# Performance work log

Hardware: AMD Instinct MI355X
Metric: run time of the kernel (lower is better)

The kernel has to match this reference:

```python
import jax, jax.numpy as jnp
import numpy as np

B, T, C, H = 4, 2048, 1024, 16
D = C // H  # head dim = 64


def setup_inputs() -> dict:
    key = jax.random.key(0)
    ks = jax.random.split(key, 5)
    s = 1.0 / np.sqrt(C)
    return {
        "x": jax.random.normal(ks[0], (B, T, C), dtype=jnp.float32),
        "Wq": jax.random.normal(ks[1], (C, C), dtype=jnp.float32) * s,
        "bq": jnp.zeros((C,), dtype=jnp.float32),
        "Wk": jax.random.normal(ks[2], (C, C), dtype=jnp.float32) * s,
        "bk": jnp.zeros((C,), dtype=jnp.float32),
        "Wv": jax.random.normal(ks[3], (C, C), dtype=jnp.float32) * s,
        "bv": jnp.zeros((C,), dtype=jnp.float32),
        "Wp": jax.random.normal(ks[4], (C, C), dtype=jnp.float32) * s,
        "bp": jnp.zeros((C,), dtype=jnp.float32),
    }


def reference(x, Wq, bq, Wk, bk, Wv, bv, Wp, bp):
    Bb, Tt, Cc = x.shape
    # QKV projections (torch Linear: y = x @ W.T + b)
    q = (x @ Wq.T + bq).reshape(Bb, Tt, H, D).transpose(0, 2, 1, 3)  # [B,H,T,D]
    k = (x @ Wk.T + bk).reshape(Bb, Tt, H, D).transpose(0, 2, 1, 3)
    v = (x @ Wv.T + bv).reshape(Bb, Tt, H, D).transpose(0, 2, 1, 3)
    att = jnp.einsum("bhqd,bhkd->bhqk", q, k) / jnp.sqrt(jnp.float32(D))
    causal = jnp.tril(jnp.ones((Tt, Tt), dtype=bool))
    att = jnp.where(causal[None, None], att, -jnp.inf)
    att = jax.nn.softmax(att, axis=-1)
    y = jnp.einsum("bhqk,bhkd->bhqd", att, v)  # [B,H,T,D]
    y = y.transpose(0, 2, 1, 3).reshape(Bb, Tt, Cc)
    return y @ Wp.T + bp
```

## Files before the change

### kernel.cpp

```cpp
#include <hip/hip_runtime.h>

typedef unsigned short u16;
typedef unsigned int u32;

typedef __attribute__((ext_vector_type(4))) float f32x4;
typedef __attribute__((ext_vector_type(8))) short bf16x8;


__device__ inline u16 f2b(float f) {
  union { float f; u32 u; } x; x.f = f;
  u32 u = x.u;
  u32 r = (u + 0x7fffu + ((u >> 16) & 1u)) >> 16;
  return (u16)r;
}

__device__ inline u32 cvtpk(float lo, float hi) {
  u32 r;
  asm("v_cvt_pk_bf16_f32 %0, %1, %2" : "=v"(r) : "v"(lo), "v"(hi));
  return r;
}

__device__ inline void gload_lds16(const void* g, void* l) {
  __builtin_amdgcn_global_load_lds(
      (const __attribute__((address_space(1))) u32*)g,
      (__attribute__((address_space(3))) u32*)l, 16, 0, 0);
}


__global__ __launch_bounds__(256) void cvt_all(const float* __restrict__ x,
                                               const float* __restrict__ w0,
                                               const float* __restrict__ w1,
                                               const float* __restrict__ w2,
                                               const float* __restrict__ w3,
                                               u16* __restrict__ xo,
                                               u16* __restrict__ wo) {
  int b = blockIdx.x;
  const float* s;
  u16* d;
  int i;
  if (b < 8192) {
    s = x; d = xo; i = b * 256 + threadIdx.x;
  } else {
    int m = (b - 8192) >> 10;
    s = (m == 0) ? w0 : (m == 1) ? w1 : (m == 2) ? w2 : w3;
    d = wo + (size_t)m * 1048576;
    i = ((b - 8192) & 1023) * 256 + threadIdx.x;
  }
  float4 v = ((const float4*)s)[i];
  ushort4 o;
  o.x = f2b(v.x); o.y = f2b(v.y); o.z = f2b(v.z); o.w = f2b(v.w);
  ((ushort4*)d)[i] = o;
}


__global__ __launch_bounds__(256) void gemm_qkv(const u16* __restrict__ A,
                                                const u16* __restrict__ W,
                                                const float* __restrict__ bq,
                                                const float* __restrict__ bk,
                                                const float* __restrict__ bv,
                                                u16* __restrict__ outQ,
                                                u16* __restrict__ outK,
                                                u16* __restrict__ outVt,
                                                float qscale) {
  __shared__ u16 sA[128 * 32];
  __shared__ u16 sB[128 * 32];

  const int K = 1024;
  const int t = threadIdx.x;
  const int lane = t & 63;
  const int w = t >> 6;
  const int wr = w >> 1, wc = w & 1;
  const int lr = lane & 15, lg = lane >> 4;

  int bid = blockIdx.y * 24 + blockIdx.x;
  int swz = (bid & 7) * 192 + (bid >> 3);
  const int mBase = (swz / 24) * 128;
  const int nBase = (swz % 24) * 128;

  f32x4 zero = {0.f, 0.f, 0.f, 0.f};
  f32x4 acc[4][4];
#pragma unroll
  for (int i = 0; i < 4; ++i)
#pragma unroll
    for (int j = 0; j < 4; ++j) acc[i][j] = zero;

  const int rA = t >> 2;
  const int cA = (t & 3) * 8;

  for (int k0 = 0; k0 < K; k0 += 32) {
#pragma unroll
    for (int i = 0; i < 2; ++i) {
      gload_lds16(A + (size_t)(mBase + i * 64 + rA) * K + k0 + cA,
                  &sA[i * 2048 + t * 8]);
      gload_lds16(W + (size_t)(nBase + i * 64 + rA) * K + k0 + cA,
                  &sB[i * 2048 + t * 8]);
    }
    __syncthreads();

    bf16x8 af[4], bf[4];
#pragma unroll
    for (int i = 0; i < 4; ++i)
      af[i] = *(const bf16x8*)&sA[(wr * 64 + i * 16 + lr) * 32 + lg * 8];
#pragma unroll
    for (int j = 0; j < 4; ++j)
      bf[j] = *(const bf16x8*)&sB[(wc * 64 + j * 16 + lr) * 32 + lg * 8];

#pragma unroll
    for (int i = 0; i < 4; ++i)
#pragma unroll
      for (int j = 0; j < 4; ++j)
        acc[i][j] = __builtin_amdgcn_mfma_f32_16x16x32_bf16(af[i], bf[j],
                                                            acc[i][j], 0, 0, 0);
    __syncthreads();
  }

  const int mode = nBase >> 10;
  const float* bias = (mode == 0) ? bq : (mode == 1) ? bk : bv;

#pragma unroll
  for (int i = 0; i < 4; ++i) {
    int row = mBase + wr * 64 + i * 16 + lg * 4;
    int b = row >> 11, tp = row & 2047;
#pragma unroll
    for (int j = 0; j < 4; ++j) {
      int col = nBase + wc * 64 + j * 16 + lr;
      int ncol = col & 1023;
      int h = ncol >> 6, dd = ncol & 63;
      float bv_ = bias[ncol];
      size_t bhOff = (size_t)(b * 16 + h) * 262144;
      if (mode == 2) {
        ushort4 o;
        o.x = f2b(acc[i][j][0] + bv_);
        o.y = f2b(acc[i][j][1] + bv_);
        o.z = f2b(acc[i][j][2] + bv_);
        o.w = f2b(acc[i][j][3] + bv_);
        *(ushort4*)((char*)outVt + bhOff + (tp >> 6) * 8192 + dd * 128 +
                    ((((tp & 63) >> 3) << 4) ^ ((dd & 7) << 4)) +
                    (tp & 7) * 2) = o;
      } else if (mode == 0) {
#pragma unroll
        for (int r = 0; r < 4; ++r)
          outQ[(((size_t)(b * 16 + h) * 2048) + tp + r) * 64 + dd] =
              f2b((acc[i][j][r] + bv_) * qscale);
      } else {
#pragma unroll
        for (int r = 0; r < 4; ++r) {
          int tt = tp + r;
          *(u16*)((char*)outK + bhOff + (tt >> 6) * 8192 + (tt & 63) * 128 +
                  (((dd >> 3) << 4) ^ ((tt & 7) << 4)) + (dd & 7) * 2) =
              f2b(acc[i][j][r] + bv_);
        }
      }
    }
  }
}


__global__ __launch_bounds__(256) void gemm_proj(const u16* __restrict__ A,
                                                 const u16* __restrict__ W,
                                                 const float* __restrict__ bias,
                                                 float* __restrict__ outF) {
  __shared__ u16 sA[128 * 32];
  __shared__ u16 sB[128 * 32];

  const int K = 1024, N = 1024;
  const int t = threadIdx.x;
  const int lane = t & 63;
  const int w = t >> 6;
  const int wr = w >> 1, wc = w & 1;
  const int lr = lane & 15, lg = lane >> 4;

  int bid = blockIdx.y * 8 + blockIdx.x;
  int swz = (bid & 7) * 64 + (bid >> 3);
  const int mBase = (swz >> 3) * 128;
  const int nBase = (swz & 7) * 128;

  f32x4 zero = {0.f, 0.f, 0.f, 0.f};
  f32x4 acc[4][4];
#pragma unroll
  for (int i = 0; i < 4; ++i)
#pragma unroll
    for (int j = 0; j < 4; ++j) acc[i][j] = zero;

  const int rA = t >> 2;
  const int cA = (t & 3) * 8;

  for (int k0 = 0; k0 < K; k0 += 32) {
#pragma unroll
    for (int i = 0; i < 2; ++i) {
      gload_lds16(A + (size_t)(mBase + i * 64 + rA) * K + k0 + cA,
                  &sA[i * 2048 + t * 8]);
      gload_lds16(W + (size_t)(nBase + i * 64 + rA) * K + k0 + cA,
                  &sB[i * 2048 + t * 8]);
    }
    __syncthreads();

    bf16x8 af[4], bf[4];
#pragma unroll
    for (int i = 0; i < 4; ++i)
      af[i] = *(const bf16x8*)&sA[(wr * 64 + i * 16 + lr) * 32 + lg * 8];
#pragma unroll
    for (int j = 0; j < 4; ++j)
      bf[j] = *(const bf16x8*)&sB[(wc * 64 + j * 16 + lr) * 32 + lg * 8];

#pragma unroll
    for (int i = 0; i < 4; ++i)
#pragma unroll
      for (int j = 0; j < 4; ++j)
        acc[i][j] = __builtin_amdgcn_mfma_f32_16x16x32_bf16(af[i], bf[j],
                                                            acc[i][j], 0, 0, 0);
    __syncthreads();
  }

#pragma unroll
  for (int i = 0; i < 4; ++i) {
    int row = mBase + wr * 64 + i * 16 + lg * 4;
#pragma unroll
    for (int j = 0; j < 4; ++j) {
      int col = nBase + wc * 64 + j * 16 + lr;
      float bv = bias[col];
#pragma unroll
      for (int r = 0; r < 4; ++r)
        outF[(size_t)(row + r) * N + col] = acc[i][j][r] + bv;
    }
  }
}


__global__ __launch_bounds__(512) void attn_fwd(const u16* __restrict__ qg,
                                                const u16* __restrict__ kswz,
                                                const u16* __restrict__ vswz,
                                                u16* __restrict__ yg) {
  __shared__ u16 sK[2][64 * 64];
  __shared__ u16 sVt[2][64 * 64];

  const int t = threadIdx.x;
  const int lane = t & 63;
  const int w = t >> 6;
  const int lr = lane & 15, lg = lane >> 4;
  const int xk = (lr & 7) << 4;

  int bid0 = blockIdx.y * 8 + blockIdx.x;
  int swzb = (bid0 & 7) * 64 + (bid0 >> 3);
  const int bh = swzb >> 3;
  const int pair = swzb & 7;

  const char* kgb = (const char*)kswz + (size_t)bh * 262144;
  const char* vgb = (const char*)vswz + (size_t)bh * 262144;
  const u16* qb = qg + (size_t)bh * 131072;

  gload_lds16(kgb + t * 16, (char*)&sK[0][0] + t * 16);
  gload_lds16(vgb + t * 16, (char*)&sVt[0][0] + t * 16);

  f32x4 zero = {0.f, 0.f, 0.f, 0.f};
  const int b = bh >> 4, h = bh & 15;
  int tc = 0;

  for (int half = 0; half < 2; ++half) {
    const int qt = half ? pair : 15 - pair;
    const int nkt = 2 * qt + 2;
    const int wq0 = qt * 128 + w * 16;
    const int qrow = wq0 + lr;

    bf16x8 qf[2];
#pragma unroll
    for (int kk = 0; kk < 2; ++kk)
      qf[kk] = *(const bf16x8*)(qb + (size_t)qrow * 64 + kk * 32 + lg * 8);

    f32x4 accO[4];
#pragma unroll
    for (int n = 0; n < 4; ++n) accO[n] = zero;
    float lrun = 0.f;

    for (int kt = 0; kt < nkt; ++kt, ++tc) {
      const int cur = tc & 1;
      __syncthreads();

      int nextT = (kt + 1 < nkt) ? kt + 1 : (half == 0 ? 0 : -1);
      if (nextT >= 0) {
        gload_lds16(kgb + nextT * 8192 + t * 16,
                    (char*)&sK[cur ^ 1][0] + t * 16);
        gload_lds16(vgb + nextT * 8192 + t * 16,
                    (char*)&sVt[cur ^ 1][0] + t * 16);
      }

      if (kt * 64 > wq0 + 15) continue;

      const char* kb_ = (const char*)&sK[cur][0];
      const char* vb_ = (const char*)&sVt[cur][0];

      f32x4 s[4];
      __builtin_amdgcn_s_setprio(1);
#pragma unroll
      for (int n = 0; n < 4; ++n) {
        f32x4 a = zero;
#pragma unroll
        for (int kk = 0; kk < 2; ++kk) {
          bf16x8 kf = *(const bf16x8*)(kb_ + (n * 16 + lr) * 128 +
                                       ((kk * 64 + lg * 16) ^ xk));
          a = __builtin_amdgcn_mfma_f32_16x16x32_bf16(kf, qf[kk], a, 0, 0, 0);
        }
        s[n] = a;
      }
      __builtin_amdgcn_s_setprio(0);

      if (kt * 64 + 63 > wq0) {
#pragma unroll
        for (int n = 0; n < 4; ++n) {
          int key0 = kt * 64 + n * 16 + lg * 4;
#pragma unroll
          for (int r = 0; r < 4; ++r)
            s[n][r] = (key0 + r <= qrow) ? s[n][r] : -1e30f;
        }
      }

      u32 pk[4][2];
#pragma unroll
      for (int n = 0; n < 4; ++n) {
        float p0 = exp2f(s[n][0] - 12.f);
        float p1 = exp2f(s[n][1] - 12.f);
        float p2 = exp2f(s[n][2] - 12.f);
        float p3 = exp2f(s[n][3] - 12.f);
        lrun += (p0 + p1) + (p2 + p3);
        pk[n][0] = cvtpk(p0, p1);
        pk[n][1] = cvtpk(p2, p3);
      }

      const bool hi = (lg >> 1) & 1;
#pragma unroll
      for (int kk = 0; kk < 2; ++kk) {
        u32 g[4];
#pragma unroll
        for (int r = 0; r < 4; ++r) {
          const int rh = r >> 1, rl = r & 1;
          u32 give = ((lg & 1) ^ rh) ? pk[2 * kk + 1][rl] : pk[2 * kk][rl];
          int srcLane = ((lg & 1) * 2 + ((lg >> 1) ^ rh)) * 16 + lr;
          g[r] = (u32)__shfl((int)give, srcLane);
        }
        union { u32 u[4]; bf16x8 v; } pu;
        pu.u[0] = hi ? g[2] : g[0];
        pu.u[1] = hi ? g[3] : g[1];
        pu.u[2] = hi ? g[0] : g[2];
        pu.u[3] = hi ? g[1] : g[3];
        bf16x8 pf = pu.v;
        __builtin_amdgcn_s_setprio(1);
#pragma unroll
        for (int n = 0; n < 4; ++n) {
          bf16x8 vf = *(const bf16x8*)(vb_ + (n * 16 + lr) * 128 +
                                       ((kk * 64 + lg * 16) ^ xk));
          accO[n] = __builtin_amdgcn_mfma_f32_16x16x32_bf16(pf, vf, accO[n], 0, 0, 0);
        }
        __builtin_amdgcn_s_setprio(0);
      }
    }

    lrun += __shfl_xor(lrun, 16);
    lrun += __shfl_xor(lrun, 32);

#pragma unroll
    for (int r = 0; r < 4; ++r) {
      float linv = 1.f / __shfl(lrun, lg * 4 + r);
      int trow = qt * 128 + w * 16 + lg * 4 + r;
      size_t rowOff = ((size_t)b * 2048 + trow) * 1024 + h * 64;
#pragma unroll
      for (int n = 0; n < 4; ++n)
        yg[rowOff + n * 16 + lr] = f2b(accO[n][r] * linv);
    }
  }
}


extern "C" void kernel_launch(void* const* d_in, const int* in_sizes, int n_in,
                              void* d_out, int out_size, void* d_ws, size_t ws_size,
                              hipStream_t stream) {
  const float* x  = (const float*)d_in[0];
  const float* Wq = (const float*)d_in[1];
  const float* bq = (const float*)d_in[2];
  const float* Wk = (const float*)d_in[3];
  const float* bk = (const float*)d_in[4];
  const float* Wv = (const float*)d_in[5];
  const float* bv = (const float*)d_in[6];
  const float* Wp = (const float*)d_in[7];
  const float* bp = (const float*)d_in[8];
  float* out = (float*)d_out;

  char* ws = (char*)d_ws;
  u16* xb  = (u16*)(ws);
  u16* wqb = (u16*)(ws + (16u << 20));
  u16* wpb = (u16*)(ws + (22u << 20));
  u16* qb  = (u16*)(ws + (24u << 20));
  u16* kb  = (u16*)(ws + (40u << 20));
  u16* vtb = (u16*)(ws + (56u << 20));
  u16* yb  = (u16*)(ws + (72u << 20));

  const float SCL = 0.18033688011112042f;

  cvt_all<<<12288, 256, 0, stream>>>(x, Wq, Wk, Wv, Wp, xb, wqb);

  gemm_qkv<<<dim3(24, 64), 256, 0, stream>>>(xb, wqb, bq, bk, bv,
                                             qb, kb, vtb, SCL);

  attn_fwd<<<dim3(8, 64), 512, 0, stream>>>(qb, kb, vtb, yb);

  gemm_proj<<<dim3(8, 64), 256, 0, stream>>>(yb, wpb, bp, out);
}
```

Before: 189.5 us.

## Double-buffer GEMM LDS tiles with 256x128 tiles and 512-thread blocks

Both the QKV and output-projection GEMMs move to 512-thread blocks computing 256x128 tiles. The K loop is now double-buffered so the next K-slice is loaded into LDS while MFMAs run on the current one, with one barrier per iteration instead of two. MFMA issue is wrapped in s_setprio. For the Q and K outputs the MFMA operands are swapped so each lane holds four consecutive head-dim values, letting the epilogue write vectorized ushort4 stores and load float4 bias instead of scattered scalar u16 stores. The tradeoff is more LDS and register pressure per block, and half as many blocks, which could reduce occupancy or CU coverage.

```diff
diff --git a/kernel.cpp b/kernel.cpp
--- a/kernel.cpp
+++ b/kernel.cpp
@@ -53,7 +53,7 @@
 }
 
 
-__global__ __launch_bounds__(256) void gemm_qkv(const u16* __restrict__ A,
+__global__ __launch_bounds__(512) void gemm_qkv(const u16* __restrict__ A,
                                                 const u16* __restrict__ W,
                                                 const float* __restrict__ bq,
                                                 const float* __restrict__ bk,
@@ -62,8 +62,8 @@
                                                 u16* __restrict__ outK,
                                                 u16* __restrict__ outVt,
                                                 float qscale) {
-  __shared__ u16 sA[128 * 32];
-  __shared__ u16 sB[128 * 32];
+  __shared__ u16 sA[2][256 * 32];
+  __shared__ u16 sB[2][128 * 32];
 
   const int K = 1024;
   const int t = threadIdx.x;
@@ -73,9 +73,10 @@
   const int lr = lane & 15, lg = lane >> 4;
 
   int bid = blockIdx.y * 24 + blockIdx.x;
-  int swz = (bid & 7) * 192 + (bid >> 3);
-  const int mBase = (swz / 24) * 128;
+  int swz = (bid & 7) * 96 + (bid >> 3);
+  const int mBase = (swz / 24) * 256;
   const int nBase = (swz % 24) * 128;
+  const int mode = nBase >> 10;
 
   f32x4 zero = {0.f, 0.f, 0.f, 0.f};
   f32x4 acc[4][4];
@@ -87,48 +88,61 @@
   const int rA = t >> 2;
   const int cA = (t & 3) * 8;
 
+  auto stage = [&](int buf, int k0) {
+    gload_lds16(A + (size_t)(mBase + rA) * K + k0 + cA, &sA[buf][t * 8]);
+    gload_lds16(A + (size_t)(mBase + 128 + rA) * K + k0 + cA,
+                &sA[buf][4096 + t * 8]);
+    gload_lds16(W + (size_t)(nBase + rA) * K + k0 + cA, &sB[buf][t * 8]);
+  };
+
+  stage(0, 0);
+  __syncthreads();
+  int cur = 0;
+
   for (int k0 = 0; k0 < K; k0 += 32) {
-#pragma unroll
-    for (int i = 0; i < 2; ++i) {
-      gload_lds16(A + (size_t)(mBase + i * 64 + rA) * K + k0 + cA,
-                  &sA[i * 2048 + t * 8]);
-      gload_lds16(W + (size_t)(nBase + i * 64 + rA) * K + k0 + cA,
-                  &sB[i * 2048 + t * 8]);
-    }
+    if (k0 + 32 < K) stage(cur ^ 1, k0 + 32);
+
+    bf16x8 af[4], bf[4];
+#pragma unroll
+    for (int i = 0; i < 4; ++i)
+      af[i] = *(const bf16x8*)&sA[cur][(wr * 64 + i * 16 + lr) * 32 + lg * 8];
+#pragma unroll
+    for (int j = 0; j < 4; ++j)
+      bf[j] = *(const bf16x8*)&sB[cur][(wc * 64 + j * 16 + lr) * 32 + lg * 8];
+
+    __builtin_amdgcn_s_setprio(1);
+    if (mode == 2) {
+#pragma unroll
+      for (int i = 0; i < 4; ++i)
+#pragma unroll
+        for (int j = 0; j < 4; ++j)
+          acc[i][j] = __builtin_amdgcn_mfma_f32_16x16x32_bf16(af[i], bf[j],
+                                                              acc[i][j], 0, 0, 0);
+    } else {
+#pragma unroll
+      for (int i = 0; i < 4; ++i)
+#pragma unroll
+        for (int j = 0; j < 4; ++j)
+          acc[i][j] = __builtin_amdgcn_mfma_f32_16x16x32_bf16(bf[j], af[i],
+                                                              acc[i][j], 0, 0, 0);
+    }
+    __builtin_amdgcn_s_setprio(0);
+
     __syncthreads();
-
-    bf16x8 af[4], bf[4];
-#pragma unroll
-    for (int i = 0; i < 4; ++i)
-      af[i] = *(const bf16x8*)&sA[(wr * 64 + i * 16 + lr) * 32 + lg * 8];
-#pragma unroll
-    for (int j = 0; j < 4; ++j)
-      bf[j] = *(const bf16x8*)&sB[(wc * 64 + j * 16 + lr) * 32 + lg * 8];
-
-#pragma unroll
-    for (int i = 0; i < 4; ++i)
-#pragma unroll
-      for (int j = 0; j < 4; ++j)
-        acc[i][j] = __builtin_amdgcn_mfma_f32_16x16x32_bf16(af[i], bf[j],
-                                                            acc[i][j], 0, 0, 0);
-    __syncthreads();
-  }
-
-  const int mode = nBase >> 10;
-  const float* bias = (mode == 0) ? bq : (mode == 1) ? bk : bv;
-
-#pragma unroll
-  for (int i = 0; i < 4; ++i) {
-    int row = mBase + wr * 64 + i * 16 + lg * 4;
-    int b = row >> 11, tp = row & 2047;
-#pragma unroll
-    for (int j = 0; j < 4; ++j) {
-      int col = nBase + wc * 64 + j * 16 + lr;
-      int ncol = col & 1023;
-      int h = ncol >> 6, dd = ncol & 63;
-      float bv_ = bias[ncol];
-      size_t bhOff = (size_t)(b * 16 + h) * 262144;
-      if (mode == 2) {
+    cur ^= 1;
+  }
+
+  if (mode == 2) {
+#pragma unroll
+    for (int i = 0; i < 4; ++i) {
+      int row = mBase + wr * 64 + i * 16 + lg * 4;
+      int b = row >> 11, tp = row & 2047;
+#pragma unroll
+      for (int j = 0; j < 4; ++j) {
+        int ncol = (nBase + wc * 64 + j * 16 + lr) & 1023;
+        int h = ncol >> 6, dd = ncol & 63;
+        float bv_ = bv[ncol];
+        size_t bhOff = (size_t)(b * 16 + h) * 262144;
         ushort4 o;
         o.x = f2b(acc[i][j][0] + bv_);
         o.y = f2b(acc[i][j][1] + bv_);
@@ -137,18 +151,31 @@
         *(ushort4*)((char*)outVt + bhOff + (tp >> 6) * 8192 + dd * 128 +
                     ((((tp & 63) >> 3) << 4) ^ ((dd & 7) << 4)) +
                     (tp & 7) * 2) = o;
-      } else if (mode == 0) {
-#pragma unroll
-        for (int r = 0; r < 4; ++r)
-          outQ[(((size_t)(b * 16 + h) * 2048) + tp + r) * 64 + dd] =
-              f2b((acc[i][j][r] + bv_) * qscale);
-      } else {
-#pragma unroll
-        for (int r = 0; r < 4; ++r) {
-          int tt = tp + r;
-          *(u16*)((char*)outK + bhOff + (tt >> 6) * 8192 + (tt & 63) * 128 +
-                  (((dd >> 3) << 4) ^ ((tt & 7) << 4)) + (dd & 7) * 2) =
-              f2b(acc[i][j][r] + bv_);
+      }
+    }
+  } else {
+    const float* bias = (mode == 0) ? bq : bk;
+    const float scl = (mode == 0) ? qscale : 1.f;
+#pragma unroll
+    for (int i = 0; i < 4; ++i) {
+      int tt = mBase + wr * 64 + i * 16 + lr;
+      int b = tt >> 11, tp = tt & 2047;
+#pragma unroll
+      for (int j = 0; j < 4; ++j) {
+        int n0 = ((nBase + wc * 64 + j * 16) & 1023) + lg * 4;
+        int h = n0 >> 6, dd = n0 & 63;
+        float4 bi = *(const float4*)&bias[n0];
+        ushort4 o;
+        o.x = f2b((acc[i][j][0] + bi.x) * scl);
+        o.y = f2b((acc[i][j][1] + bi.y) * scl);
+        o.z = f2b((acc[i][j][2] + bi.z) * scl);
+        o.w = f2b((acc[i][j][3] + bi.w) * scl);
+        if (mode == 0) {
+          *(ushort4*)(outQ + ((size_t)(b * 16 + h) * 2048 + tp) * 64 + dd) = o;
+        } else {
+          *(ushort4*)((char*)outK + (size_t)(b * 16 + h) * 262144 +
+                      (tp >> 6) * 8192 + (tp & 63) * 128 +
+                      (((dd >> 3) << 4) ^ ((tp & 7) << 4)) + (dd & 7) * 2) = o;
         }
       }
     }
@@ -156,12 +183,12 @@
 }
 
 
-__global__ __launch_bounds__(256) void gemm_proj(const u16* __restrict__ A,
+__global__ __launch_bounds__(512) void gemm_proj(const u16* __restrict__ A,
                                                  const u16* __restrict__ W,
                                                  const float* __restrict__ bias,
                                                  float* __restrict__ outF) {
-  __shared__ u16 sA[128 * 32];
-  __shared__ u16 sB[128 * 32];
+  __shared__ u16 sA[2][256 * 32];
+  __shared__ u16 sB[2][128 * 32];
 
   const int K = 1024, N = 1024;
   const int t = threadIdx.x;
@@ -171,8 +198,8 @@
   const int lr = lane & 15, lg = lane >> 4;
 
   int bid = blockIdx.y * 8 + blockIdx.x;
-  int swz = (bid & 7) * 64 + (bid >> 3);
-  const int mBase = (swz >> 3) * 128;
+  int swz = (bid & 7) * 32 + (bid >> 3);
+  const int mBase = (swz >> 3) * 256;
   const int nBase = (swz & 7) * 128;
 
   f32x4 zero = {0.f, 0.f, 0.f, 0.f};
@@ -185,31 +212,39 @@
   const int rA = t >> 2;
   const int cA = (t & 3) * 8;
 
+  auto stage = [&](int buf, int k0) {
+    gload_lds16(A + (size_t)(mBase + rA) * K + k0 + cA, &sA[buf][t * 8]);
+    gload_lds16(A + (size_t)(mBase + 128 + rA) * K + k0 + cA,
+                &sA[buf][4096 + t * 8]);
+    gload_lds16(W + (size_t)(nBase + rA) * K + k0 + cA, &sB[buf][t * 8]);
+  };
+
+  stage(0, 0);
+  __syncthreads();
+  int cur = 0;
+
   for (int k0 = 0; k0 < K; k0 += 32) {
-#pragma unroll
-    for (int i = 0; i < 2; ++i) {
-      gload_lds16(A + (size_t)(mBase + i * 64 + rA) * K + k0 + cA,
-                  &sA[i * 2048 + t * 8]);
-      gload_lds16(W + (size_t)(nBase + i * 64 + rA) * K + k0 + cA,
-                  &sB[i * 2048 + t * 8]);
-    }
-    __syncthreads();
+    if (k0 + 32 < K) stage(cur ^ 1, k0 + 32);
 
     bf16x8 af[4], bf[4];
 #pragma unroll
     for (int i = 0; i < 4; ++i)
-      af[i] = *(const bf16x8*)&sA[(wr * 64 + i * 16 + lr) * 32 + lg * 8];
+      af[i] = *(const bf16x8*)&sA[cur][(wr * 64 + i * 16 + lr) * 32 + lg * 8];
 #pragma unroll
     for (int j = 0; j < 4; ++j)
-      bf[j] = *(const bf16x8*)&sB[(wc * 64 + j * 16 + lr) * 32 + lg * 8];
-
+      bf[j] = *(const bf16x8*)&sB[cur][(wc * 64 + j * 16 + lr) * 32 + lg * 8];
+
+    __builtin_amdgcn_s_setprio(1);
 #pragma unroll
     for (int i = 0; i < 4; ++i)
 #pragma unroll
       for (int j = 0; j < 4; ++j)
         acc[i][j] = __builtin_amdgcn_mfma_f32_16x16x32_bf16(af[i], bf[j],
                                                             acc[i][j], 0, 0, 0);
+    __builtin_amdgcn_s_setprio(0);
+
     __syncthreads();
+    cur ^= 1;
   }
 
 #pragma unroll
@@ -397,10 +432,10 @@
 
   cvt_all<<<12288, 256, 0, stream>>>(x, Wq, Wk, Wv, Wp, xb, wqb);
 
-  gemm_qkv<<<dim3(24, 64), 256, 0, stream>>>(xb, wqb, bq, bk, bv,
+  gemm_qkv<<<dim3(24, 32), 512, 0, stream>>>(xb, wqb, bq, bk, bv,
                                              qb, kb, vtb, SCL);
 
   attn_fwd<<<dim3(8, 64), 512, 0, stream>>>(qb, kb, vtb, yb);
 
-  gemm_proj<<<dim3(8, 64), 256, 0, stream>>>(yb, wpb, bp, out);
-}
+  gemm_proj<<<dim3(8, 32), 512, 0, stream>>>(yb, wpb, bp, out);
+}
```

Measured after the change: 214.5 us. +13.2%, slower.

## Transpose MFMA operands for Q/K to vectorize stores and remap XCD tiles

Applied to the files above, without the earlier changes.

For the Q and K tiles, the QKV GEMM swaps the MFMA A/B operands so each lane holds four consecutive head-dim values. The epilogue can then write ushort4 vector stores with float4 bias loads instead of scalar u16 scatter stores. The block-to-tile mapping is also changed so each XCD owns three N column tiles across all M rows, and the projection GEMM drops its swizzle for a plain row-major mapping. The aim is to cut uncoalesced store traffic and improve L2 locality of weights per XCD, at the risk of worse locality for the activation tiles.

```diff
diff --git a/kernel.cpp b/kernel.cpp
--- a/kernel.cpp
+++ b/kernel.cpp
@@ -73,16 +73,17 @@
   const int lr = lane & 15, lg = lane >> 4;
 
   int bid = blockIdx.y * 24 + blockIdx.x;
-  int swz = (bid & 7) * 192 + (bid >> 3);
-  const int mBase = (swz / 24) * 128;
-  const int nBase = (swz % 24) * 128;
+  int xcd = bid & 7, j = bid >> 3;
+  const int mBase = (j & 63) * 128;
+  const int nBase = (xcd * 3 + (j >> 6)) * 128;
+  const int mode = nBase >> 10;
 
   f32x4 zero = {0.f, 0.f, 0.f, 0.f};
   f32x4 acc[4][4];
 #pragma unroll
   for (int i = 0; i < 4; ++i)
 #pragma unroll
-    for (int j = 0; j < 4; ++j) acc[i][j] = zero;
+    for (int jj = 0; jj < 4; ++jj) acc[i][jj] = zero;
 
   const int rA = t >> 2;
   const int cA = (t & 3) * 8;
@@ -102,53 +103,71 @@
     for (int i = 0; i < 4; ++i)
       af[i] = *(const bf16x8*)&sA[(wr * 64 + i * 16 + lr) * 32 + lg * 8];
 #pragma unroll
-    for (int j = 0; j < 4; ++j)
-      bf[j] = *(const bf16x8*)&sB[(wc * 64 + j * 16 + lr) * 32 + lg * 8];
-
-#pragma unroll
-    for (int i = 0; i < 4; ++i)
-#pragma unroll
-      for (int j = 0; j < 4; ++j)
-        acc[i][j] = __builtin_amdgcn_mfma_f32_16x16x32_bf16(af[i], bf[j],
-                                                            acc[i][j], 0, 0, 0);
+    for (int jj = 0; jj < 4; ++jj)
+      bf[jj] = *(const bf16x8*)&sB[(wc * 64 + jj * 16 + lr) * 32 + lg * 8];
+
+    if (mode == 2) {
+#pragma unroll
+      for (int i = 0; i < 4; ++i)
+#pragma unroll
+        for (int jj = 0; jj < 4; ++jj)
+          acc[i][jj] = __builtin_amdgcn_mfma_f32_16x16x32_bf16(af[i], bf[jj],
+                                                               acc[i][jj], 0, 0, 0);
+    } else {
+#pragma unroll
+      for (int i = 0; i < 4; ++i)
+#pragma unroll
+        for (int jj = 0; jj < 4; ++jj)
+          acc[i][jj] = __builtin_amdgcn_mfma_f32_16x16x32_bf16(bf[jj], af[i],
+                                                               acc[i][jj], 0, 0, 0);
+    }
     __syncthreads();
   }
 
-  const int mode = nBase >> 10;
-  const float* bias = (mode == 0) ? bq : (mode == 1) ? bk : bv;
-
-#pragma unroll
-  for (int i = 0; i < 4; ++i) {
-    int row = mBase + wr * 64 + i * 16 + lg * 4;
-    int b = row >> 11, tp = row & 2047;
-#pragma unroll
-    for (int j = 0; j < 4; ++j) {
-      int col = nBase + wc * 64 + j * 16 + lr;
-      int ncol = col & 1023;
-      int h = ncol >> 6, dd = ncol & 63;
-      float bv_ = bias[ncol];
-      size_t bhOff = (size_t)(b * 16 + h) * 262144;
-      if (mode == 2) {
+  if (mode == 2) {
+#pragma unroll
+    for (int i = 0; i < 4; ++i) {
+      int row = mBase + wr * 64 + i * 16 + lg * 4;
+      int b = row >> 11, tp = row & 2047;
+#pragma unroll
+      for (int jj = 0; jj < 4; ++jj) {
+        int ncol = (nBase + wc * 64 + jj * 16 + lr) & 1023;
+        int h = ncol >> 6, dd = ncol & 63;
+        float bv_ = bv[ncol];
+        size_t bhOff = (size_t)(b * 16 + h) * 262144;
         ushort4 o;
-        o.x = f2b(acc[i][j][0] + bv_);
-        o.y = f2b(acc[i][j][1] + bv_);
-        o.z = f2b(acc[i][j][2] + bv_);
-        o.w = f2b(acc[i][j][3] + bv_);
+        o.x = f2b(acc[i][jj][0] + bv_);
+        o.y = f2b(acc[i][jj][1] + bv_);
+        o.z = f2b(acc[i][jj][2] + bv_);
+        o.w = f2b(acc[i][jj][3] + bv_);
         *(ushort4*)((char*)outVt + bhOff + (tp >> 6) * 8192 + dd * 128 +
                     ((((tp & 63) >> 3) << 4) ^ ((dd & 7) << 4)) +
                     (tp & 7) * 2) = o;
-      } else if (mode == 0) {
-#pragma unroll
-        for (int r = 0; r < 4; ++r)
-          outQ[(((size_t)(b * 16 + h) * 2048) + tp + r) * 64 + dd] =
-              f2b((acc[i][j][r] + bv_) * qscale);
-      } else {
-#pragma unroll
-        for (int r = 0; r < 4; ++r) {
-          int tt = tp + r;
-          *(u16*)((char*)outK + bhOff + (tt >> 6) * 8192 + (tt & 63) * 128 +
-                  (((dd >> 3) << 4) ^ ((tt & 7) << 4)) + (dd & 7) * 2) =
-              f2b(acc[i][j][r] + bv_);
+      }
+    }
+  } else {
+    const float* bias = (mode == 0) ? bq : bk;
+    const float scl = (mode == 0) ? qscale : 1.f;
+#pragma unroll
+    for (int i = 0; i < 4; ++i) {
+      int tt = mBase + wr * 64 + i * 16 + lr;
+      int b = tt >> 11, tp = tt & 2047;
+#pragma unroll
+      for (int jj = 0; jj < 4; ++jj) {
+        int n0 = ((nBase + wc * 64 + jj * 16) & 1023) + lg * 4;
+        int h = n0 >> 6, dd = n0 & 63;
+        float4 bi = *(const float4*)&bias[n0];
+        ushort4 o;
+        o.x = f2b((acc[i][jj][0] + bi.x) * scl);
+        o.y = f2b((acc[i][jj][1] + bi.y) * scl);
+        o.z = f2b((acc[i][jj][2] + bi.z) * scl);
+        o.w = f2b((acc[i][jj][3] + bi.w) * scl);
+        if (mode == 0) {
+          *(ushort4*)(outQ + ((size_t)(b * 16 + h) * 2048 + tp) * 64 + dd) = o;
+        } else {
+          *(ushort4*)((char*)outK + (size_t)(b * 16 + h) * 262144 +
+                      (tp >> 6) * 8192 + (tp & 63) * 128 +
+                      (((dd >> 3) << 4) ^ ((tp & 7) << 4)) + (dd & 7) * 2) = o;
         }
       }
     }
@@ -171,9 +190,8 @@
   const int lr = lane & 15, lg = lane >> 4;
 
   int bid = blockIdx.y * 8 + blockIdx.x;
-  int swz = (bid & 7) * 64 + (bid >> 3);
-  const int mBase = (swz >> 3) * 128;
-  const int nBase = (swz & 7) * 128;
+  const int mBase = (bid >> 3) * 128;
+  const int nBase = (bid & 7) * 128;
 
   f32x4 zero = {0.f, 0.f, 0.f, 0.f};
   f32x4 acc[4][4];
```

Result: slower. 222.0 us (+17.1%).
